# Optimization experiments

Measured on AMD Instinct MI355X. Metric: run time of the kernel, lower is better.

Reference implementation:

```python
import jax, jax.numpy as jnp
import numpy as np

BN_EPS = 1e-5

@jax.custom_vjp
def bsign(x):
    # forward: sign(x) (torch semantics: sign(0)=0, matched by jnp.sign)
    return jnp.sign(x)

def _bsign_fwd(x):
    return jnp.sign(x), x

def _bsign_bwd(x, g):
    # straight-through estimator: pass grad where |x| <= 1, zero elsewhere
    return (g * (jnp.abs(x) <= 1.0).astype(g.dtype),)

bsign.defvjp(_bsign_fwd, _bsign_bwd)


def setup_inputs() -> dict:
    key = jax.random.key(0)
    k1, k2 = jax.random.split(key, 2)
    B, IN, OUT = 8192, 2048, 2048
    x = jax.random.normal(k1, (B, IN), dtype=jnp.float32)
    weight = jax.random.normal(k2, (OUT, IN), dtype=jnp.float32) * 0.1
    gamma = jnp.ones((OUT,), dtype=jnp.float32)
    beta = jnp.zeros((OUT,), dtype=jnp.float32)
    return {"x": x, "weight": weight, "gamma": gamma, "beta": beta}


def reference(x, weight, gamma, beta):
    # binarize input and weight to {-1, 0, +1} via sign (STE in bwd)
    xb = bsign(x)            # [B, IN]
    wb = bsign(weight)       # [OUT, IN]
    out = xb @ wb.T          # [B, OUT] full-precision GEMM over +/-1 values
    # BatchNorm1d, training mode: normalize with biased batch statistics
    mean = jnp.mean(out, axis=0)                 # [OUT]
    var = jnp.var(out, axis=0)                   # biased (ddof=0), matches torch BN
    out = (out - mean) * jax.lax.rsqrt(var + BN_EPS) * gamma + beta
    return out
```

## Files before the change

### kernel.cpp

```cpp
#include <hip/hip_runtime.h>
#include <stdint.h>


typedef int int32x4 __attribute__((ext_vector_type(4)));

#define BM 128
#define BN 128
#define BKI 128
#define EPS_BN 1e-5f
#define BAR_STRIDE 32

__device__ __forceinline__ void load16_lds(const void* g, void* l) {
  __builtin_amdgcn_global_load_lds(
      (const __attribute__((address_space(1))) void*)g,
      (__attribute__((address_space(3))) void*)l,
      16, 0, 0);
}

__device__ __forceinline__ char sgn(float v) {
  return v > 0.f ? (char)1 : (v < 0.f ? (char)-1 : (char)0);
}

__global__ void binarize_kernel(const float* __restrict__ x,
                                const float* __restrict__ w,
                                char* __restrict__ Ab, char* __restrict__ Bb,
                                float* __restrict__ stats,
                                int nx4, int ntot4, int n2) {
  int idx = blockIdx.x * blockDim.x + threadIdx.x;
  if (idx < n2) stats[idx] = 0.f;
  if (idx >= ntot4) return;
  const float4* src;
  char* dst;
  int i;
  if (idx < nx4) {
    src = reinterpret_cast<const float4*>(x); dst = Ab; i = idx;
  } else {
    src = reinterpret_cast<const float4*>(w); dst = Bb; i = idx - nx4;
  }
  float4 v = src[i];
  char4 o;
  o.x = sgn(v.x); o.y = sgn(v.y); o.z = sgn(v.z); o.w = sgn(v.w);
  reinterpret_cast<char4*>(dst)[i] = o;
}

__global__ __launch_bounds__(256, 4) void gemm_bn_kernel(
    const char* __restrict__ A,
    const char* __restrict__ Bt,
    float* __restrict__ C,
    float* __restrict__ colSum,
    float* __restrict__ colSq,
    int* __restrict__ barriers,
    const float* __restrict__ gamma,
    const float* __restrict__ beta,
    int M, int N, int K) {
  __shared__ __align__(16) char sA[BM * BKI];
  __shared__ __align__(16) char sB[BN * BKI];

  const int tid  = threadIdx.x;
  const int wave = tid >> 6;
  const int lane = tid & 63;

  const int nby = M / BM;
  const int panel = blockIdx.x / nby;
  const int rowBlock = (blockIdx.x % nby) * BM;
  const int colBlock = panel * BN;

  const int laneRow = lane >> 3;
  const int c       = lane & 7;
  const int swz     = ((c ^ laneRow) & 7) * 16;

  const char* Ag = A  + (size_t)(rowBlock + wave * 32 + laneRow) * K + swz;
  const char* Bg = Bt + (size_t)(colBlock + wave * 32 + laneRow) * K + swz;
  char* sAw = &sA[(wave * 32) * BKI];
  char* sBw = &sB[(wave * 32) * BKI];

  const int f    = lane & 15;
  const int quad = lane >> 4;
  const int wr = (wave >> 1) * 64;
  const int wc = (wave & 1) * 64;
  const int f7 = f & 7;

  int32x4 acc[4][4] = {};

  for (int k0 = 0; k0 < K; k0 += BKI) {
    __syncthreads();
#pragma unroll
    for (int i = 0; i < 4; ++i) {
      load16_lds(Ag + k0 + (size_t)(i * 8) * K, sAw + i * 8 * BKI);
      load16_lds(Bg + k0 + (size_t)(i * 8) * K, sBw + i * 8 * BKI);
    }
    __syncthreads();

#pragma unroll
    for (int s = 0; s < 2; ++s) {
      const int chunk = ((s * 4 + quad) ^ f7) * 16;
      int32x4 af[4], bfr[4];
#pragma unroll
      for (int mi = 0; mi < 4; ++mi)
        af[mi] = *reinterpret_cast<const int32x4*>(
            &sA[(wr + mi * 16 + f) * BKI + chunk]);
#pragma unroll
      for (int ni = 0; ni < 4; ++ni)
        bfr[ni] = *reinterpret_cast<const int32x4*>(
            &sB[(wc + ni * 16 + f) * BKI + chunk]);
#pragma unroll
      for (int mi = 0; mi < 4; ++mi)
#pragma unroll
        for (int ni = 0; ni < 4; ++ni)
          acc[mi][ni] = __builtin_amdgcn_mfma_i32_16x16x64_i8(
              af[mi], bfr[ni], acc[mi][ni], 0, 0, 0);
    }
  }

#pragma unroll
  for (int ni = 0; ni < 4; ++ni) {
    const int col = colBlock + wc + ni * 16 + f;
    float s = 0.f, sq = 0.f;
#pragma unroll
    for (int mi = 0; mi < 4; ++mi)
#pragma unroll
      for (int r = 0; r < 4; ++r) {
        const float fv = (float)acc[mi][ni][r];
        s += fv;
        sq += fv * fv;
      }
    s  += __shfl_xor(s, 16);  s  += __shfl_xor(s, 32);
    sq += __shfl_xor(sq, 16); sq += __shfl_xor(sq, 32);
    if (quad == 0) {
      atomicAdd(&colSum[col], s);
      atomicAdd(&colSq[col], sq);
    }
  }

  float gmv = 0.f, btv = 0.f;
  if (tid < BN) {
    gmv = gamma[colBlock + tid];
    btv = beta[colBlock + tid];
  }

  __syncthreads();
  if (tid == 0) {
    int* bar = barriers + panel * BAR_STRIDE;
    __hip_atomic_fetch_add(bar, 1, __ATOMIC_RELAXED,
                           __HIP_MEMORY_SCOPE_AGENT);
    while (__hip_atomic_load(bar, __ATOMIC_RELAXED,
                             __HIP_MEMORY_SCOPE_AGENT) < nby) {
      __builtin_amdgcn_s_sleep(8);
    }
    asm volatile("" ::: "memory");
  }
  __syncthreads();

  float2* sSC = reinterpret_cast<float2*>(sA);
  if (tid < BN) {
    const int col = colBlock + tid;
    const float s  = __hip_atomic_load(&colSum[col], __ATOMIC_RELAXED,
                                       __HIP_MEMORY_SCOPE_AGENT);
    const float sq = __hip_atomic_load(&colSq[col], __ATOMIC_RELAXED,
                                       __HIP_MEMORY_SCOPE_AGENT);
    const float invM = 1.0f / (float)M;
    const float mu  = s * invM;
    const float var = sq * invM - mu * mu;
    const float sc  = gmv * rsqrtf(var + EPS_BN);
    const float sh  = btv - mu * sc;
    sSC[tid] = make_float2(sc, sh);
  }
  __syncthreads();

#pragma unroll
  for (int ni = 0; ni < 4; ++ni) {
    const int lc  = wc + ni * 16 + f;
    const float2 ss = sSC[lc];
    const int col = colBlock + lc;
#pragma unroll
    for (int mi = 0; mi < 4; ++mi) {
      float* Cp = C + (size_t)(rowBlock + wr + mi * 16 + quad * 4) * N + col;
#pragma unroll
      for (int r = 0; r < 4; ++r)
        Cp[(size_t)r * N] = (float)acc[mi][ni][r] * ss.x + ss.y;
    }
  }
}

extern "C" void kernel_launch(void* const* d_in, const int* in_sizes, int n_in,
                              void* d_out, int out_size, void* d_ws,
                              size_t ws_size, hipStream_t stream) {
  const float* x     = (const float*)d_in[0];
  const float* w     = (const float*)d_in[1];
  const float* gamma = (const float*)d_in[2];
  const float* beta  = (const float*)d_in[3];
  float* C = (float*)d_out;

  const int N = in_sizes[2];
  const int K = in_sizes[1] / N;
  const int M = in_sizes[0] / K;

  char* ws = (char*)d_ws;
  char* Abin = ws;
  char* Bbin = ws + (size_t)M * K;
  float* stats = (float*)(ws + (size_t)M * K + (size_t)N * K);
  float* colSum = stats;
  float* colSq  = stats + N;
  int* barriers = (int*)(stats + 2 * N);

  {
    int nx4 = (M * K) / 4;
    int ntot4 = (M * K + N * K) / 4;
    binarize_kernel<<<(ntot4 + 255) / 256, 256, 0, stream>>>(
        x, w, Abin, Bbin, stats, nx4, ntot4, 2 * N + 16 * BAR_STRIDE);
  }

  {
    const int nTiles = (M / BM) * (N / BN);
    gemm_bn_kernel<<<nTiles, 256, 0, stream>>>(Abin, Bbin, C, colSum, colSq,
                                               barriers, gamma, beta, M, N, K);
  }
}
```

Baseline: 172.0 us.

## Double-buffer LDS with 256x256 tiles and interleaved prefetch in binary GEMM

Block tiles grow from 128x128 to 256x256 with 512 threads, so each wave computes a 128x64 sub-tile. The A/B tiles for the next K step are now loaded into a second LDS buffer while MFMAs run on the current one. The compute is split into four phases separated by s_barrier, with s_setprio raised around the MFMA work. This aims to hide global-to-LDS latency and raise operand reuse, at the cost of 128KB of LDS, one block per CU, and a grid of only 256 blocks that must all be resident for the per-panel spin barrier.

Measured after the change: 165.1 us. 1.04x faster.

```diff
diff --git a/kernel.cpp b/kernel.cpp
--- a/kernel.cpp
+++ b/kernel.cpp
@@ -4,8 +4,8 @@
 
 typedef int int32x4 __attribute__((ext_vector_type(4)));
 
-#define BM 128
-#define BN 128
+#define BM 256
+#define BN 256
 #define BKI 128
 #define EPS_BN 1e-5f
 #define BAR_STRIDE 32
@@ -43,7 +43,7 @@
   reinterpret_cast<char4*>(dst)[i] = o;
 }
 
-__global__ __launch_bounds__(256, 4) void gemm_bn_kernel(
+__global__ __launch_bounds__(512, 2) void gemm_bn_kernel(
     const char* __restrict__ A,
     const char* __restrict__ Bt,
     float* __restrict__ C,
@@ -53,8 +53,8 @@
     const float* __restrict__ gamma,
     const float* __restrict__ beta,
     int M, int N, int K) {
-  __shared__ __align__(16) char sA[BM * BKI];
-  __shared__ __align__(16) char sB[BN * BKI];
+  __shared__ __align__(16) char sA[2][BM * BKI];
+  __shared__ __align__(16) char sB[2][BN * BKI];
 
   const int tid  = threadIdx.x;
   const int wave = tid >> 6;
@@ -66,61 +66,104 @@
   const int colBlock = panel * BN;
 
   const int laneRow = lane >> 3;
-  const int c       = lane & 7;
-  const int swz     = ((c ^ laneRow) & 7) * 16;
+  const int cch     = lane & 7;
+  const int swz     = ((cch ^ laneRow) & 7) * 16;
 
   const char* Ag = A  + (size_t)(rowBlock + wave * 32 + laneRow) * K + swz;
   const char* Bg = Bt + (size_t)(colBlock + wave * 32 + laneRow) * K + swz;
-  char* sAw = &sA[(wave * 32) * BKI];
-  char* sBw = &sB[(wave * 32) * BKI];
 
   const int f    = lane & 15;
   const int quad = lane >> 4;
-  const int wr = (wave >> 1) * 64;
-  const int wc = (wave & 1) * 64;
-  const int f7 = f & 7;
-
-  int32x4 acc[4][4] = {};
-
-  for (int k0 = 0; k0 < K; k0 += BKI) {
+  const int f7   = f & 7;
+  const int wm = (wave >> 2) * 128;
+  const int wn = (wave & 3) * 64;
+
+  int32x4 acc[8][4] = {};
+
+  const int NT = K / BKI;
+
+#pragma unroll
+  for (int j = 0; j < 4; ++j) {
+    load16_lds(Ag + (size_t)(j * 8) * K, &sA[0][(wave * 32 + j * 8) * BKI]);
+    load16_lds(Bg + (size_t)(j * 8) * K, &sB[0][(wave * 32 + j * 8) * BKI]);
+  }
+
+  for (int t = 0; t < NT; ++t) {
+    const int cur = t & 1;
+    const int nxt = cur ^ 1;
+    const char* sAc = sA[cur];
+    const char* sBc = sB[cur];
+    const size_t gkn = (size_t)(t + 1) * BKI;
+    const bool pre = (t + 1 < NT);
+
     __syncthreads();
-#pragma unroll
-    for (int i = 0; i < 4; ++i) {
-      load16_lds(Ag + k0 + (size_t)(i * 8) * K, sAw + i * 8 * BKI);
-      load16_lds(Bg + k0 + (size_t)(i * 8) * K, sBw + i * 8 * BKI);
-    }
-    __syncthreads();
-
-#pragma unroll
-    for (int s = 0; s < 2; ++s) {
-      const int chunk = ((s * 4 + quad) ^ f7) * 16;
-      int32x4 af[4], bfr[4];
+
+    int32x4 af[4][2];
+#pragma unroll
+    for (int q = 0; q < 4; ++q) {
+      const int mh = q >> 1, nh = q & 1;
+      if (nh == 0) {
+#pragma unroll
+        for (int mi = 0; mi < 4; ++mi)
+#pragma unroll
+          for (int s = 0; s < 2; ++s)
+            af[mi][s] = *reinterpret_cast<const int32x4*>(
+                &sAc[(wm + mh * 64 + mi * 16 + f) * BKI +
+                     (((s * 4 + quad) ^ f7) * 16)]);
+      }
+      int32x4 bf_[2][2];
+#pragma unroll
+      for (int ni = 0; ni < 2; ++ni)
+#pragma unroll
+        for (int s = 0; s < 2; ++s)
+          bf_[ni][s] = *reinterpret_cast<const int32x4*>(
+              &sBc[(wn + nh * 32 + ni * 16 + f) * BKI +
+                   (((s * 4 + quad) ^ f7) * 16)]);
+
+      if (pre) {
+        if (q < 2) {
+#pragma unroll
+          for (int j = 0; j < 2; ++j) {
+            const int part = q * 2 + j;
+            load16_lds(Ag + gkn + (size_t)(part * 8) * K,
+                       &sA[nxt][(wave * 32 + part * 8) * BKI]);
+          }
+        } else {
+#pragma unroll
+          for (int j = 0; j < 2; ++j) {
+            const int part = (q - 2) * 2 + j;
+            load16_lds(Bg + gkn + (size_t)(part * 8) * K,
+                       &sB[nxt][(wave * 32 + part * 8) * BKI]);
+          }
+        }
+      }
+
+      __builtin_amdgcn_s_barrier();
+      __builtin_amdgcn_s_setprio(1);
 #pragma unroll
       for (int mi = 0; mi < 4; ++mi)
-        af[mi] = *reinterpret_cast<const int32x4*>(
-            &sA[(wr + mi * 16 + f) * BKI + chunk]);
-#pragma unroll
-      for (int ni = 0; ni < 4; ++ni)
-        bfr[ni] = *reinterpret_cast<const int32x4*>(
-            &sB[(wc + ni * 16 + f) * BKI + chunk]);
-#pragma unroll
-      for (int mi = 0; mi < 4; ++mi)
-#pragma unroll
-        for (int ni = 0; ni < 4; ++ni)
-          acc[mi][ni] = __builtin_amdgcn_mfma_i32_16x16x64_i8(
-              af[mi], bfr[ni], acc[mi][ni], 0, 0, 0);
-    }
-  }
-
-#pragma unroll
-  for (int ni = 0; ni < 4; ++ni) {
-    const int col = colBlock + wc + ni * 16 + f;
+#pragma unroll
+        for (int ni = 0; ni < 2; ++ni)
+#pragma unroll
+          for (int s = 0; s < 2; ++s)
+            acc[mh * 4 + mi][nh * 2 + ni] =
+                __builtin_amdgcn_mfma_i32_16x16x64_i8(
+                    af[mi][s], bf_[ni][s], acc[mh * 4 + mi][nh * 2 + ni],
+                    0, 0, 0);
+      __builtin_amdgcn_s_setprio(0);
+      __builtin_amdgcn_s_barrier();
+    }
+  }
+
+#pragma unroll
+  for (int in = 0; in < 4; ++in) {
+    const int col = colBlock + wn + in * 16 + f;
     float s = 0.f, sq = 0.f;
 #pragma unroll
-    for (int mi = 0; mi < 4; ++mi)
+    for (int im = 0; im < 8; ++im)
 #pragma unroll
       for (int r = 0; r < 4; ++r) {
-        const float fv = (float)acc[mi][ni][r];
+        const float fv = (float)acc[im][in][r];
         s += fv;
         sq += fv * fv;
       }
@@ -151,7 +194,7 @@
   }
   __syncthreads();
 
-  float2* sSC = reinterpret_cast<float2*>(sA);
+  float2* sSC = reinterpret_cast<float2*>(&sA[0][0]);
   if (tid < BN) {
     const int col = colBlock + tid;
     const float s  = __hip_atomic_load(&colSum[col], __ATOMIC_RELAXED,
@@ -168,16 +211,16 @@
   __syncthreads();
 
 #pragma unroll
-  for (int ni = 0; ni < 4; ++ni) {
-    const int lc  = wc + ni * 16 + f;
+  for (int in = 0; in < 4; ++in) {
+    const int lc  = wn + in * 16 + f;
     const float2 ss = sSC[lc];
     const int col = colBlock + lc;
 #pragma unroll
-    for (int mi = 0; mi < 4; ++mi) {
-      float* Cp = C + (size_t)(rowBlock + wr + mi * 16 + quad * 4) * N + col;
+    for (int im = 0; im < 8; ++im) {
+      float* Cp = C + (size_t)(rowBlock + wm + im * 16 + quad * 4) * N + col;
 #pragma unroll
       for (int r = 0; r < 4; ++r)
-        Cp[(size_t)r * N] = (float)acc[mi][ni][r] * ss.x + ss.y;
+        Cp[(size_t)r * N] = (float)acc[im][in][r] * ss.x + ss.y;
     }
   }
 }
@@ -212,7 +255,7 @@
 
   {
     const int nTiles = (M / BM) * (N / BN);
-    gemm_bn_kernel<<<nTiles, 256, 0, stream>>>(Abin, Bbin, C, colSum, colSq,
+    gemm_bn_kernel<<<nTiles, 512, 0, stream>>>(Abin, Bbin, C, colSum, colSq,
                                                barriers, gamma, beta, M, N, K);
   }
 }
```
